# Optimization experiments

Measured on AMD Instinct MI355X. Metric: run time of the kernel, lower is better.

The kernel has to match this reference:

```python
import jax, jax.numpy as jnp
import numpy as np

H, D = 16, 64  # num_head, num_out
LN_EPS = 1e-5

def setup_inputs() -> dict:
    key = jax.random.key(0)
    ks = jax.random.split(key, 6)
    B, S, C = 4, 2048, 1024
    sc = 0.02
    return {
        "x": jax.random.normal(ks[0], (B, S, C), jnp.float32),
        "mask": jax.random.randint(ks[1], (B, S), 0, 2, jnp.int32),
        "Wq": jax.random.normal(ks[2], (C, C), jnp.float32) * sc,
        "Wk": jax.random.normal(ks[3], (C, C), jnp.float32) * sc,
        "Wv": jax.random.normal(ks[4], (C, C), jnp.float32) * sc,
        "Wr": jax.random.normal(ks[5], (C, C), jnp.float32) * sc,
        "gamma": jnp.ones((C,), jnp.float32),
        "beta": jnp.zeros((C,), jnpip := jnp.float32) if False else jnp.zeros((C,), jnp.float32),
    }

def reference(x, mask, Wq, Wk, Wv, Wr, gamma, beta):
    B, S, C = x.shape
    # torch Linear: y = x @ W.T ; split(num_out,-1) == reshape (B,S,H,D)
    q = (x @ Wq.T).reshape(B, S, H, D)
    k = (x @ Wk.T).reshape(B, S, H, D)
    v = (x @ Wv.T).reshape(B, S, H, D)
    scores = jnp.einsum("bqhd,bkhd->bhqk", q, k) / jnp.sqrt(jnp.float32(D))
    # mask [B,S] over keys; masked positions -> -1e9 (matches masked_fill)
    scores = jnp.where((mask == 0)[:, None, None, :], jnp.float32(-1e9), scores)
    attn = jax.nn.softmax(scores, axis=-1)
    out = jnp.einsum("bhqk,bkhd->bqhd", attn, v).reshape(B, S, H * D)
    out = jax.nn.relu(out + x @ Wr.T)
    mu = jnp.mean(out, axis=-1, keepdims=True)
    var = jnp.mean(jnp.square(out - mu), axis=-1, keepdims=True)
    return (out - mu) / jnp.sqrt(var + LN_EPS) * gamma + beta
```

## Files before the change

kernel.cpp:

```cpp
#include <hip/hip_runtime.h>

typedef __attribute__((ext_vector_type(8))) short short8;
typedef __attribute__((ext_vector_type(4))) float f32x4;
typedef __attribute__((ext_vector_type(4))) unsigned short u16x4;
typedef __attribute__((ext_vector_type(4))) float float4v;

#define MFMA(a, b, c) __builtin_amdgcn_mfma_f32_16x16x32_bf16(a, b, c, 0, 0, 0)
#define GLOAD_LDS16(gp, lp) __builtin_amdgcn_global_load_lds( \
    (const __attribute__((address_space(1))) void*)(gp),      \
    (__attribute__((address_space(3))) void*)(lp), 16, 0, 0)

__device__ __forceinline__ float bf2f(unsigned short u) {
    union { unsigned int i; float f; } v; v.i = ((unsigned int)u) << 16; return v.f;
}
__device__ __forceinline__ unsigned short f2bf(float f) {
    union { float f; unsigned int i; } v; v.f = f;
    unsigned int r = (v.i + 0x7FFFu + ((v.i >> 16) & 1u)) >> 16;
    return (unsigned short)r;
}
__device__ __forceinline__ unsigned short f2bfr(float f) {
    union { float f; unsigned int i; } v; v.f = f;
    return (unsigned short)((v.i + 0x8000u) >> 16);
}

__global__ __launch_bounds__(256)
void mask_scan(const int* __restrict__ mask, int* __restrict__ rmap, int* __restrict__ seff)
{
    constexpr int S = 2048;
    const int b = blockIdx.x;
    const int tid = threadIdx.x;
    __shared__ int ps[256];
    const int* m = mask + b * S;
    int loc[8], s = 0;
#pragma unroll
    for (int j = 0; j < 8; ++j) { loc[j] = m[tid * 8 + j]; s += loc[j]; }
    ps[tid] = s;
    __syncthreads();
    for (int off = 1; off < 256; off <<= 1) {
        int v = (tid >= off) ? ps[tid - off] : 0;
        __syncthreads();
        ps[tid] += v;
        __syncthreads();
    }
    int run = (tid > 0) ? ps[tid - 1] : 0;
#pragma unroll
    for (int j = 0; j < 8; ++j) {
        rmap[b * S + tid * 8 + j] = loc[j] ? (b * S + run) : -1;
        run += loc[j];
    }
    if (tid == 255) seff[b] = ps[255];
}

__global__ __launch_bounds__(256)
void ingest(const float* __restrict__ src, unsigned short* __restrict__ dst, int n4)
{
    const int stride = gridDim.x * blockDim.x;
    for (int i = blockIdx.x * blockDim.x + threadIdx.x; i < n4; i += stride) {
        float4v v = ((const float4v*)src)[i];
        u16x4 o;
#pragma unroll
        for (int j = 0; j < 4; ++j) o[j] = f2bf(v[j]);
        ((u16x4*)dst)[i] = o;
    }
}

__global__ __launch_bounds__(256)
void proj_gemm(const unsigned short* __restrict__ X,
               const unsigned short* __restrict__ Wq, const unsigned short* __restrict__ Wk,
               const unsigned short* __restrict__ Wv, const unsigned short* __restrict__ Wr,
               unsigned short* __restrict__ Qo, unsigned short* __restrict__ Ko,
               unsigned short* __restrict__ Vo, unsigned short* __restrict__ Ro,
               const int* __restrict__ rmap)
{
    constexpr int Kd = 1024, N = 1024;
    __shared__ unsigned short As[128 * 32];
    __shared__ unsigned short Bs[128 * 32];
    const int tid = threadIdx.x;
    const int wid = tid >> 6, lane = tid & 63;
    const int g = lane >> 4, lr = lane & 15;
    const int wsel = blockIdx.z;
    const unsigned short* W = (wsel == 0) ? Wq : (wsel == 1) ? Wk : (wsel == 2) ? Wv : Wr;
    unsigned short* O = (wsel == 0) ? Qo : (wsel == 1) ? Ko : (wsel == 2) ? Vo : Ro;
    const bool compact = (wsel == 1) || (wsel == 2);
    const int rowBase = blockIdx.x * 128;
    const int colBase = blockIdx.y * 128;
    const int wm = wid >> 1, wn = wid & 1;

    f32x4 acc[4][4] = {};

    const int r0 = tid >> 2;
    const int c0 = (tid & 3) * 8;
    const unsigned short* ga0 = X + (size_t)(rowBase + r0) * Kd + c0;
    const unsigned short* ga1 = X + (size_t)(rowBase + 64 + r0) * Kd + c0;
    const unsigned short* gb0 = W + (size_t)(colBase + r0) * Kd + c0;
    const unsigned short* gb1 = W + (size_t)(colBase + 64 + r0) * Kd + c0;

    for (int kt = 0; kt < Kd; kt += 32) {
        if (kt) __syncthreads();
        GLOAD_LDS16(ga0 + kt, As + (size_t)tid * 8);
        GLOAD_LDS16(ga1 + kt, As + 2048 + (size_t)tid * 8);
        GLOAD_LDS16(gb0 + kt, Bs + (size_t)tid * 8);
        GLOAD_LDS16(gb1 + kt, Bs + 2048 + (size_t)tid * 8);
        asm volatile("s_waitcnt vmcnt(0)" ::: "memory");
        __syncthreads();
        short8 a[4], b[4];
#pragma unroll
        for (int mt = 0; mt < 4; ++mt)
            a[mt] = *reinterpret_cast<const short8*>(&As[(wm * 64 + mt * 16 + lr) * 32 + g * 8]);
#pragma unroll
        for (int nt = 0; nt < 4; ++nt)
            b[nt] = *reinterpret_cast<const short8*>(&Bs[(wn * 64 + nt * 16 + lr) * 32 + g * 8]);
#pragma unroll
        for (int mt = 0; mt < 4; ++mt)
#pragma unroll
            for (int nt = 0; nt < 4; ++nt)
                acc[mt][nt] = MFMA(a[mt], b[nt], acc[mt][nt]);
    }
#pragma unroll
    for (int mt = 0; mt < 4; ++mt)
#pragma unroll
        for (int nt = 0; nt < 4; ++nt)
#pragma unroll
            for (int r = 0; r < 4; ++r) {
                int row = rowBase + wm * 64 + mt * 16 + g * 4 + r;
                int col = colBase + wn * 64 + nt * 16 + lr;
                if (compact) {
                    int orow = rmap[row];
                    if (orow >= 0) O[(size_t)orow * N + col] = f2bf(acc[mt][nt][r]);
                } else {
                    O[(size_t)row * N + col] = f2bf(acc[mt][nt][r]);
                }
            }
}

__global__ __launch_bounds__(512)
void attn_fwd(const unsigned short* __restrict__ Q, const unsigned short* __restrict__ Kb,
              const unsigned short* __restrict__ Vb, const int* __restrict__ seff,
              unsigned short* __restrict__ AO)
{
    constexpr int S = 2048, C = 1024, Dh = 64;
    constexpr int PST = 64;
    constexpr float SCL = 0.125f * 1.44269504f;
    constexpr float FM  = 16.0f;
    constexpr float MSK = -1.0e30f;
    __shared__ unsigned short Kt[2][64 * 64];
    __shared__ unsigned short Vt[2][64 * 64];
    __shared__ unsigned short Pt[8][16 * PST];
    const int tid = threadIdx.x;
    const int w = tid >> 6, lane = tid & 63;
    const int g = lane >> 4, lr = lane & 15;
    const int lin = blockIdx.x;
    const int hb = lin & 63, qt = lin >> 6;
    const int h = hb >> 2, b = hb & 3;
    const int qbase = qt * 128;
    const int qrow = qbase + w * 16 + lr;

    const int Sb = seff[b];
    const int ntiles = (Sb + 63) >> 6;

    const unsigned short* qptr = Q + (size_t)(b * S + qrow) * C + h * Dh;
    short8 qf[2];
    qf[0] = *reinterpret_cast<const short8*>(qptr + g * 8);
    qf[1] = *reinterpret_cast<const short8*>(qptr + 32 + g * 8);

    short8 ones;
#pragma unroll
    for (int j = 0; j < 8; ++j) ones[j] = (short)0x3F80;

    f32x4 o[4] = {};
    f32x4 lacc = {};

    const unsigned short* kg = Kb + (size_t)(b * S) * C + h * Dh;
    const unsigned short* vg = Vb + (size_t)(b * S) * C + h * Dh;

    const int kk0 = tid >> 3;
    const int kd0 = ((tid & 7) ^ (kk0 & 7)) * 8;
    const int vkey = tid >> 3;
    const int vsd = (tid & 7) * 8;

    short8 vv;
    GLOAD_LDS16(kg + (size_t)kk0 * C + kd0, &Kt[0][(size_t)tid * 8]);
    vv = *reinterpret_cast<const short8*>(vg + (size_t)vkey * C + vsd);
    asm volatile("s_waitcnt vmcnt(0)" ::: "memory");
    {
        const unsigned short* bb = (const unsigned short*)&vv;
#pragma unroll
        for (int j = 0; j < 8; ++j) {
            int d = vsd + j;
            int sw = (d & 7) ^ ((d >> 3) & 7);
            Vt[0][d * 64 + ((((vkey >> 3) ^ sw) << 3) | (vkey & 7))] = bb[j];
        }
    }
    __syncthreads();

    int cur = 0;
    for (int tt = 0; tt < ntiles; ++tt) {
        const int t = tt * 64;
        const bool hasNext = (tt + 1) < ntiles;
        if (hasNext) {
            const int tn = t + 64;
            GLOAD_LDS16(kg + (size_t)(tn + kk0) * C + kd0, &Kt[cur ^ 1][(size_t)tid * 8]);
            vv = *reinterpret_cast<const short8*>(vg + (size_t)(tn + vkey) * C + vsd);
        }
        f32x4 s[4];
        __builtin_amdgcn_s_setprio(1);
#pragma unroll
        for (int nt = 0; nt < 4; ++nt) {
            int key = nt * 16 + lr;
            f32x4 a = {};
#pragma unroll
            for (int c = 0; c < 2; ++c) {
                int dd = c * 32 + g * 8;
                short8 kf = *reinterpret_cast<const short8*>(
                    &Kt[cur][key * 64 + (((dd >> 3) ^ (key & 7)) << 3)]);
                a = MFMA(qf[c], kf, a);
            }
            s[nt] = a;
        }
        __builtin_amdgcn_s_setprio(0);
        float madd[4];
#pragma unroll
        for (int nt = 0; nt < 4; ++nt)
            madd[nt] = ((t + nt * 16 + lr) < Sb) ? -FM : MSK;
        unsigned short* Pw = Pt[w];
#pragma unroll
        for (int nt = 0; nt < 4; ++nt) {
            int k = nt * 16 + lr;
#pragma unroll
            for (int r = 0; r < 4; ++r) {
                float p = __builtin_amdgcn_exp2f(s[nt][r] * SCL + madd[nt]);
                int row = g * 4 + r;
                Pw[row * PST + ((((k >> 3) ^ (row & 7)) << 3) | (k & 7))] = f2bfr(p);
            }
        }
        asm volatile("s_waitcnt lgkmcnt(0)" ::: "memory");
        __builtin_amdgcn_sched_barrier(0);
        short8 pf[2];
#pragma unroll
        for (int hh = 0; hh < 2; ++hh) {
            int kk = hh * 32 + g * 8;
            pf[hh] = *reinterpret_cast<const short8*>(
                &Pw[lr * PST + (((kk >> 3) ^ (lr & 7)) << 3)]);
        }
        __builtin_amdgcn_s_setprio(1);
        lacc = MFMA(pf[0], ones, lacc);
        lacc = MFMA(pf[1], ones, lacc);
#pragma unroll
        for (int dt = 0; dt < 4; ++dt) {
            int d = dt * 16 + lr;
#pragma unroll
            for (int hh = 0; hh < 2; ++hh) {
                int kk = hh * 32 + g * 8;
                short8 vf = *reinterpret_cast<const short8*>(
                    &Vt[cur][d * 64 + ((((kk >> 3) ^ (d & 7) ^ ((d >> 3) & 7)) << 3))]);
                o[dt] = MFMA(pf[hh], vf, o[dt]);
            }
        }
        __builtin_amdgcn_s_setprio(0);
        if (hasNext) {
            asm volatile("s_waitcnt vmcnt(0)" ::: "memory");
            const unsigned short* bb = (const unsigned short*)&vv;
            unsigned short* Vn = Vt[cur ^ 1];
#pragma unroll
            for (int j = 0; j < 8; ++j) {
                int d = vsd + j;
                int sw = (d & 7) ^ ((d >> 3) & 7);
                Vn[d * 64 + ((((vkey >> 3) ^ sw) << 3) | (vkey & 7))] = bb[j];
            }
        }
        __syncthreads();
        cur ^= 1;
    }
#pragma unroll
    for (int dt = 0; dt < 4; ++dt)
#pragma unroll
        for (int r = 0; r < 4; ++r) {
            int row = qbase + w * 16 + g * 4 + r;
            int col = h * Dh + dt * 16 + lr;
            AO[(size_t)(b * S + row) * C + col] = f2bf(o[dt][r] / lacc[r]);
        }
}

__global__ __launch_bounds__(256)
void ln_ep(const unsigned short* __restrict__ AO, const unsigned short* __restrict__ R,
           const float* __restrict__ gamma, const float* __restrict__ beta,
           float* __restrict__ out)
{
    constexpr int C = 1024;
    const int row = blockIdx.x;
    const int tid = threadIdx.x;
    __shared__ float s1[256];
    __shared__ float s2[256];

    float v[4]; float sum = 0.f, ss = 0.f;
#pragma unroll
    for (int i = 0; i < 4; ++i) {
        int c = tid * 4 + i;
        float a = bf2f(AO[(size_t)row * C + c]);
        float r = bf2f(R[(size_t)row * C + c]);
        v[i] = fmaxf(0.f, a + r);
        sum += v[i]; ss += v[i] * v[i];
    }
    s1[tid] = sum; s2[tid] = ss;
    __syncthreads();
    for (int st = 128; st > 0; st >>= 1) {
        if (tid < st) { s1[tid] += s1[tid + st]; s2[tid] += s2[tid + st]; }
        __syncthreads();
    }
    float mu = s1[0] * (1.f / C);
    float var = s2[0] * (1.f / C) - mu * mu;
    float rstd = rsqrtf(var + 1e-5f);
    float4v g4 = *reinterpret_cast<const float4v*>(gamma + tid * 4);
    float4v b4 = *reinterpret_cast<const float4v*>(beta + tid * 4);
    float4v ov;
#pragma unroll
    for (int i = 0; i < 4; ++i)
        ov[i] = (v[i] - mu) * rstd * g4[i] + b4[i];
    *reinterpret_cast<float4v*>(out + (size_t)row * C + tid * 4) = ov;
}

extern "C" void kernel_launch(void* const* d_in, const int* in_sizes, int n_in,
                              void* d_out, int out_size, void* d_ws, size_t ws_size,
                              hipStream_t stream)
{
    const float* X = (const float*)d_in[0];
    const int* mask = (const int*)d_in[1];
    const float* Wq = (const float*)d_in[2];
    const float* Wk = (const float*)d_in[3];
    const float* Wv = (const float*)d_in[4];
    const float* Wr = (const float*)d_in[5];
    const float* Gm = (const float*)d_in[6];
    const float* Bt = (const float*)d_in[7];
    float* out = (float*)d_out;

    const size_t NE = (size_t)8192 * 1024;
    const size_t WE = (size_t)1024 * 1024;
    unsigned short* p = (unsigned short*)d_ws;
    unsigned short* Xb = p;   p += NE;
    unsigned short* Wqb = p;  p += WE;
    unsigned short* Wkb = p;  p += WE;
    unsigned short* Wvb = p;  p += WE;
    unsigned short* Wrb = p;  p += WE;
    unsigned short* Qb = p;   p += NE;
    unsigned short* Kb = p;   p += NE;
    unsigned short* Vb = p;   p += NE;
    unsigned short* Rb = p;   p += NE;
    int* rmap = (int*)p;      p += 8192 * 2;
    int* seff = (int*)p;      p += 8;
    unsigned short* AO = Xb;

    mask_scan<<<dim3(4), 256, 0, stream>>>(mask, rmap, seff);
    ingest<<<dim3(2048), 256, 0, stream>>>(X, Xb, (int)(NE / 4));
    ingest<<<dim3(512), 256, 0, stream>>>(Wq, Wqb, (int)(WE / 4));
    ingest<<<dim3(512), 256, 0, stream>>>(Wk, Wkb, (int)(WE / 4));
    ingest<<<dim3(512), 256, 0, stream>>>(Wv, Wvb, (int)(WE / 4));
    ingest<<<dim3(512), 256, 0, stream>>>(Wr, Wrb, (int)(WE / 4));

    proj_gemm<<<dim3(64, 8, 4), 256, 0, stream>>>(Xb, Wqb, Wkb, Wvb, Wrb,
                                                  Qb, Kb, Vb, Rb, rmap);
    attn_fwd<<<dim3(1024), 512, 0, stream>>>(Qb, Kb, Vb, seff, AO);
    ln_ep<<<dim3(8192), 256, 0, stream>>>(AO, Rb, Gm, Bt, out);
}
```

Before: 194.1 us.

## Gather unmasked key rows before K/V projection and skip empty tiles

The mask scan now builds a gather index of unmasked key positions for each batch, padded with a valid row index. The K and V projection blocks gather X rows through this index, write compacted outputs contiguously, and return early when a tile lies beyond the batch's unmasked count. This skips roughly half the K/V GEMM work on masks that are about half zeros, where before every row was computed and masked rows were dropped only at store time. The grid grows to 68 row tiles (17 per batch), and blocks that have no work exit early.

```diff
diff --git a/kernel.cpp b/kernel.cpp
--- a/kernel.cpp
+++ b/kernel.cpp
@@ -24,7 +24,7 @@
 }
 
 __global__ __launch_bounds__(256)
-void mask_scan(const int* __restrict__ mask, int* __restrict__ rmap, int* __restrict__ seff)
+void mask_scan(const int* __restrict__ mask, int* __restrict__ kidx, int* __restrict__ seff)
 {
     constexpr int S = 2048;
     const int b = blockIdx.x;
@@ -34,6 +34,8 @@
     int loc[8], s = 0;
 #pragma unroll
     for (int j = 0; j < 8; ++j) { loc[j] = m[tid * 8 + j]; s += loc[j]; }
+#pragma unroll
+    for (int j = 0; j < 8; ++j) kidx[b * S + tid * 8 + j] = b * S;
     ps[tid] = s;
     __syncthreads();
     for (int off = 1; off < 256; off <<= 1) {
@@ -45,7 +47,7 @@
     int run = (tid > 0) ? ps[tid - 1] : 0;
 #pragma unroll
     for (int j = 0; j < 8; ++j) {
-        rmap[b * S + tid * 8 + j] = loc[j] ? (b * S + run) : -1;
+        if (loc[j]) kidx[b * S + run] = b * S + tid * 8 + j;
         run += loc[j];
     }
     if (tid == 255) seff[b] = ps[255];
@@ -70,7 +72,7 @@
                const unsigned short* __restrict__ Wv, const unsigned short* __restrict__ Wr,
                unsigned short* __restrict__ Qo, unsigned short* __restrict__ Ko,
                unsigned short* __restrict__ Vo, unsigned short* __restrict__ Ro,
-               const int* __restrict__ rmap)
+               const int* __restrict__ kidx, const int* __restrict__ seff)
 {
     constexpr int Kd = 1024, N = 1024;
     __shared__ unsigned short As[128 * 32];
@@ -79,10 +81,19 @@
     const int wid = tid >> 6, lane = tid & 63;
     const int g = lane >> 4, lr = lane & 15;
     const int wsel = blockIdx.z;
+    const bool compact = (wsel == 1) || (wsel == 2);
+    int rowBase;
+    if (compact) {
+        int bx = blockIdx.x;
+        int b = bx / 17, xt = bx - b * 17;
+        if (xt * 128 >= seff[b]) return;
+        rowBase = b * 2048 + xt * 128;
+    } else {
+        if (blockIdx.x >= 64) return;
+        rowBase = blockIdx.x * 128;
+    }
     const unsigned short* W = (wsel == 0) ? Wq : (wsel == 1) ? Wk : (wsel == 2) ? Wv : Wr;
     unsigned short* O = (wsel == 0) ? Qo : (wsel == 1) ? Ko : (wsel == 2) ? Vo : Ro;
-    const bool compact = (wsel == 1) || (wsel == 2);
-    const int rowBase = blockIdx.x * 128;
     const int colBase = blockIdx.y * 128;
     const int wm = wid >> 1, wn = wid & 1;
 
@@ -90,8 +101,10 @@
 
     const int r0 = tid >> 2;
     const int c0 = (tid & 3) * 8;
-    const unsigned short* ga0 = X + (size_t)(rowBase + r0) * Kd + c0;
-    const unsigned short* ga1 = X + (size_t)(rowBase + 64 + r0) * Kd + c0;
+    const int sA0 = compact ? kidx[rowBase + r0] : rowBase + r0;
+    const int sA1 = compact ? kidx[rowBase + 64 + r0] : rowBase + 64 + r0;
+    const unsigned short* ga0 = X + (size_t)sA0 * Kd + c0;
+    const unsigned short* ga1 = X + (size_t)sA1 * Kd + c0;
     const unsigned short* gb0 = W + (size_t)(colBase + r0) * Kd + c0;
     const unsigned short* gb1 = W + (size_t)(colBase + 64 + r0) * Kd + c0;
 
@@ -124,12 +137,7 @@
             for (int r = 0; r < 4; ++r) {
                 int row = rowBase + wm * 64 + mt * 16 + g * 4 + r;
                 int col = colBase + wn * 64 + nt * 16 + lr;
-                if (compact) {
-                    int orow = rmap[row];
-                    if (orow >= 0) O[(size_t)orow * N + col] = f2bf(acc[mt][nt][r]);
-                } else {
-                    O[(size_t)row * N + col] = f2bf(acc[mt][nt][r]);
-                }
+                O[(size_t)row * N + col] = f2bf(acc[mt][nt][r]);
             }
 }
 
@@ -345,19 +353,19 @@
     unsigned short* Kb = p;   p += NE;
     unsigned short* Vb = p;   p += NE;
     unsigned short* Rb = p;   p += NE;
-    int* rmap = (int*)p;      p += 8192 * 2;
+    int* kidx = (int*)p;      p += 8192 * 2;
     int* seff = (int*)p;      p += 8;
     unsigned short* AO = Xb;
 
-    mask_scan<<<dim3(4), 256, 0, stream>>>(mask, rmap, seff);
+    mask_scan<<<dim3(4), 256, 0, stream>>>(mask, kidx, seff);
     ingest<<<dim3(2048), 256, 0, stream>>>(X, Xb, (int)(NE / 4));
     ingest<<<dim3(512), 256, 0, stream>>>(Wq, Wqb, (int)(WE / 4));
     ingest<<<dim3(512), 256, 0, stream>>>(Wk, Wkb, (int)(WE / 4));
     ingest<<<dim3(512), 256, 0, stream>>>(Wv, Wvb, (int)(WE / 4));
     ingest<<<dim3(512), 256, 0, stream>>>(Wr, Wrb, (int)(WE / 4));
 
-    proj_gemm<<<dim3(64, 8, 4), 256, 0, stream>>>(Xb, Wqb, Wkb, Wvb, Wrb,
-                                                  Qb, Kb, Vb, Rb, rmap);
+    proj_gemm<<<dim3(68, 8, 4), 256, 0, stream>>>(Xb, Wqb, Wkb, Wvb, Wrb,
+                                                  Qb, Kb, Vb, Rb, kidx, seff);
     attn_fwd<<<dim3(1024), 512, 0, stream>>>(Qb, Kb, Vb, seff, AO);
     ln_ep<<<dim3(8192), 256, 0, stream>>>(AO, Rb, Gm, Bt, out);
 }
```

New measurement: 177.2 us. 1.09x faster.
